# Optimization experiments

Measured on AMD Instinct MI355X. Metric: run time of the kernel, lower is better.

Reference implementation:

```python
import jax, jax.numpy as jnp
import numpy as np

B, T, N, C_IN = 8, 16, 2048, 2
H, C_OUT = 64, 64
KT, K = 3, 3
E = 32768


def setup_inputs() -> dict:
    key = jax.random.key(0)
    ks = jax.random.split(key, 8)
    X = jax.random.normal(ks[0], (B, T, N, C_IN), jnp.float32)
    edge_index = jax.random.randint(ks[1], (2, E), 0, N, dtype=jnp.int64)
    edge_weight = jax.random.uniform(ks[2], (E,), jnp.float32)
    conv1_w = jax.random.normal(ks[3], (2 * H, C_IN, KT, 1), jnp.float32) * 0.1
    conv1_b = jnp.zeros((2 * H,), jnp.float32)
    cheb_w = jax.random.normal(ks[4], (K, H, H), jnp.float32) * 0.05
    cheb_b = jnp.zeros((H,), jnp.float32)
    conv2_w = jax.random.normal(ks[5], (2 * C_OUT, H, KT, 1), jnp.float32) * 0.05
    conv2_b = jnp.zeros((2 * C_OUT,), jnp.float32)
    return dict(X=X, edge_index=edge_index, edge_weight=edge_weight,
                conv1_w=conv1_w, conv1_b=conv1_b, cheb_w=cheb_w, cheb_b=cheb_b,
                conv2_w=conv2_w, conv2_b=conv2_b)


def temporal_conv(x, w, b, c_out, kt):
    # x: [B, T, N, C_in] -> [B, T-kt+1, N, c_out]; causal conv (valid) + GLU with aligned residual
    xc = jnp.transpose(x, (0, 3, 1, 2))  # [B, C, T, N]
    bsz, c_in, t, n = xc.shape
    if c_in < c_out:
        x_in = jnp.concatenate([xc, jnp.zeros((bsz, c_out - c_in, t, n), xc.dtype)], axis=1)
    else:
        x_in = xc  # c_in == c_out case here (Align identity)
    x_in = x_in[:, :, kt - 1:, :]
    y = jax.lax.conv_general_dilated(xc, w, (1, 1), 'VALID',
                                     dimension_numbers=('NCHW', 'OIHW', 'NCHW'))
    y = y + b[None, :, None, None]  # [B, 2*c_out, T-kt+1, N]
    x_p, x_q = y[:, :c_out], y[:, c_out:]
    out = (x_p + x_in) * jax.nn.sigmoid(x_q)  # GLU
    return jnp.transpose(out, (0, 2, 3, 1))  # [B, T', N, c_out]


def cheb_conv(x, src, dst, ew, W, bias):
    # x: [G, N, H]. PyG ChebConv, sym normalization, lambda_max=2 =>
    # L_hat = -D^{-1/2} A D^{-1/2} with zero diagonal (self-loops removed/cancelled).
    n = x.shape[1]
    w = jnp.where(src == dst, jnp.zeros_like(ew), ew)  # remove self loops
    deg = jnp.zeros((n,), x.dtype).at[src].add(w)
    deg_safe = jnp.where(deg > 0, deg, jnp.ones_like(deg))
    dis = jnp.where(deg > 0, jax.lax.rsqrt(deg_safe), jnp.zeros_like(deg))
    wn = -dis[src] * w * dis[dst]  # scaled Laplacian edge weights

    def lhat(z):  # sparse L_hat @ z, batched over graph dim
        return jnp.zeros_like(z).at[:, dst].add(z[:, src] * wn[None, :, None])

    tx0 = x
    out = jnp.einsum('gnh,ho->gno', tx0, W[0])
    tx1 = lhat(x)
    out = out + jnp.einsum('gnh,ho->gno', tx1, W[1])
    for k in range(2, W.shape[0]):
        tx2 = 2.0 * lhat(tx1) - tx0
        out = out + jnp.einsum('gnh,ho->gno', tx2, W[k])
        tx0, tx1 = tx1, tx2
    return out + bias


def reference(X, edge_index, edge_weight, conv1_w, conv1_b, cheb_w, cheb_b, conv2_w, conv2_b):
    t0 = temporal_conv(X, conv1_w, conv1_b, H, KT)      # [B, T-2, N, H]
    bsz, tm, n, h = t0.shape
    g = t0.reshape(bsz * tm, n, h)
    src, dst = edge_index[0], edge_index[1]
    tg = cheb_conv(g, src, dst, edge_weight, cheb_w, cheb_b)
    tg = jax.nn.relu(tg).reshape(bsz, tm, n, h)
    out = temporal_conv(tg, conv2_w, conv2_b, C_OUT, KT)  # [B, T-4, N, C_OUT]
    # batch_norm=False, dropout=0 (eval): the permute pairs cancel -> identity
    return out
```

## Files before the change

kernel.cpp:

```cpp
#include <hip/hip_runtime.h>
#include <cstdint>

#define B_ 8
#define T_ 16
#define N_ 2048
#define CIN_ 2
#define H_ 64
#define COUT_ 64
#define KT_ 3
#define E_ 32768
#define T1_ 14
#define T2_ 12
#define G_ (B_*T1_)

typedef __attribute__((ext_vector_type(8))) short bf16x8;
typedef __attribute__((ext_vector_type(4))) float f32x4;
typedef unsigned short ushort_;
typedef __attribute__((ext_vector_type(8))) unsigned short u16x8;

__device__ __forceinline__ float sigmoidf_(float x){ return 1.f/(1.f+expf(-x)); }
__device__ __forceinline__ int rfl_(int x){ return __builtin_amdgcn_readfirstlane(x); }

__device__ __forceinline__ ushort_ f2b(float x){
  union {float f; uint32_t u;} v; v.f = x;
  uint32_t r = (v.u + 0x7FFFu + ((v.u>>16)&1u)) >> 16;
  return (ushort_)r;
}
__device__ __forceinline__ float b2f(ushort_ x){
  union {uint32_t u; float f;} v; v.u = ((uint32_t)x)<<16;
  return v.f;
}

__global__ void k_setup(const float* __restrict__ cw, const float* __restrict__ w2,
                        ushort_* __restrict__ Bp, ushort_* __restrict__ Bp2,
                        float* __restrict__ deg, int* __restrict__ cnt,
                        int* __restrict__ fillc){
  int bi = blockIdx.x; int tid = threadIdx.x;
  if(bi < 6){
    int i = bi*256 + tid;
    int lane = i & 63; int cn = i >> 6; int c = cn >> 2; int n = cn & 3;
    #pragma unroll
    for(int j=0;j<8;j++){
      int k = c*32 + (lane>>4)*8 + j;
      int h = k & 63; int m = k >> 6;
      int col = n*16 + (lane&15);
      float v;
      if(m == 0)      v = cw[(size_t)h*64 + col] - cw[(size_t)(128+h)*64 + col];
      else if(m == 1) v = cw[(size_t)(64+h)*64 + col];
      else            v = 2.f*cw[(size_t)(128+h)*64 + col];
      Bp[(size_t)i*8 + j] = f2b(v);
    }
  } else if(bi < 18){
    int i = (bi-6)*256 + tid;
    int lane = i & 63; int cn = i >> 6; int c = cn >> 3; int n = cn & 7;
    #pragma unroll
    for(int j=0;j<8;j++){
      int k = c*32 + (lane>>4)*8 + j;
      int co = n*16 + (lane&15);
      int kt = k >> 6, ci = k & 63;
      Bp2[(size_t)i*8 + j] = f2b(w2[(size_t)co*192 + ci*3 + kt]);
    }
  } else {
    int i = (bi-18)*256 + tid;
    if(i < N_){ deg[i] = 0.f; cnt[i] = 0; fillc[i] = 0; }
  }
}

__global__ void k_deg_cnt(const int* __restrict__ src, const int* __restrict__ dst,
                          const float* __restrict__ ew, float* deg, int* cnt){
  int e = blockIdx.x*blockDim.x + threadIdx.x;
  if(e >= E_) return;
  int s = src[e], d = dst[e];
  float w = (s==d) ? 0.f : ew[e];
  atomicAdd(&deg[s], w);
  atomicAdd(&cnt[d], 1);
}

__global__ void k_scan_dis(const int* __restrict__ cnt, int* __restrict__ offs,
                           float* __restrict__ deg){
  __shared__ int sums[256];
  int tid = threadIdx.x;
  int base = tid*8;
  int loc[8]; int s = 0;
  #pragma unroll
  for(int j=0;j<8;j++){ loc[j]=s; s += cnt[base+j]; }
  sums[tid] = s; __syncthreads();
  for(int ofs=1; ofs<256; ofs<<=1){
    int t = (tid>=ofs) ? sums[tid-ofs] : 0;
    __syncthreads();
    sums[tid] += t;
    __syncthreads();
  }
  int ebase = (tid==0) ? 0 : sums[tid-1];
  #pragma unroll
  for(int j=0;j<8;j++) offs[base+j] = ebase + loc[j];
  if(tid==255) offs[N_] = sums[255];
  #pragma unroll
  for(int j=0;j<8;j++){
    float dg = deg[base+j];
    deg[base+j] = dg > 0.f ? rsqrtf(dg) : 0.f;
  }
}

__global__ void k_fill_conv1(const int* __restrict__ src, const int* __restrict__ dst,
                             const float* __restrict__ ew, const float* __restrict__ dis,
                             const int* __restrict__ offs, int* fillc,
                             int2* __restrict__ epack,
                             const float* __restrict__ X, const float* __restrict__ w1,
                             const float* __restrict__ b1, ushort_* __restrict__ t0){
  int bi = blockIdx.x;
  if(bi < 128){
    int e = bi*256 + threadIdx.x;
    if(e >= E_) return;
    int s = src[e], d = dst[e];
    float w = (s==d) ? 0.f : ew[e];
    float wn = -dis[s]*w*dis[d];
    int pos = offs[d] + atomicAdd(&fillc[d], 1);
    epack[pos] = make_int2(s, __float_as_int(wn));
    return;
  }
  int wv = rfl_((bi-128)*4 + (threadIdx.x>>6));
  int lane = threadIdx.x & 63;
  int nb = wv % (N_/8); int bt = wv / (N_/8); int b = bt / T1_; int t = bt % T1_;
  int n0 = nb*8;
  const float* Xp = X + ((size_t)((b*T_ + t)*N_ + n0))*CIN_;
  float wp[6], wq[6];
  #pragma unroll
  for(int k=0;k<6;k++){
    wp[k] = w1[ lane      *6 + k];
    wq[k] = w1[(lane+H_)*6 + k];
  }
  float bp = b1[lane], bq = b1[lane+H_];
  ushort_* ob = t0 + ((size_t)bt*N_ + n0)*H_ + lane;
  #pragma unroll
  for(int j=0;j<8;j++){
    float yp = bp, yq = bq;
    #pragma unroll
    for(int kt=0;kt<KT_;kt++)
      #pragma unroll
      for(int ci=0;ci<CIN_;ci++){
        float x = Xp[kt*(N_*CIN_) + j*CIN_ + ci];
        yp += x * wp[ci*3+kt];
        yq += x * wq[ci*3+kt];
      }
    float xin = (lane < CIN_) ? Xp[2*(N_*CIN_) + j*CIN_ + lane] : 0.f;
    ob[j*H_] = f2b((yp + xin) * sigmoidf_(yq));
  }
}

__global__ void k_spmm3(const ushort_* __restrict__ zin, ushort_* __restrict__ out,
                        const int* __restrict__ offs, const int2* __restrict__ epack){
  int lane = threadIdx.x & 63;
  int wv = threadIdx.x >> 6;
  int bid = blockIdx.x;
  int work = (bid & 7)*896 + (bid >> 3);
  int gg = work >> 9;
  int dblk = work & 511;
  int d = dblk*4 + wv;
  int e0 = offs[d], e1 = offs[d+1];
  size_t lbase = (size_t)(gg*8 + (lane>>3))*N_*H_ + (lane&7)*8;
  const ushort_* zb = zin + lbase;
  float ac[8] = {};
  int i = e0;
  for(; i+7 < e1; i += 8){
    int2 ee[8]; u16x8 zz[8];
    #pragma unroll
    for(int u=0;u<8;u++) ee[u] = epack[i+u];
    #pragma unroll
    for(int u=0;u<8;u++) zz[u] = *(const u16x8*)(zb + (size_t)ee[u].x*H_);
    #pragma unroll
    for(int u=0;u<8;u++){
      float w = __int_as_float(ee[u].y);
      #pragma unroll
      for(int j=0;j<8;j++) ac[j] += w*b2f(zz[u][j]);
    }
  }
  for(; i+3 < e1; i += 4){
    int2 ee[4]; u16x8 zz[4];
    #pragma unroll
    for(int u=0;u<4;u++) ee[u] = epack[i+u];
    #pragma unroll
    for(int u=0;u<4;u++) zz[u] = *(const u16x8*)(zb + (size_t)ee[u].x*H_);
    #pragma unroll
    for(int u=0;u<4;u++){
      float w = __int_as_float(ee[u].y);
      #pragma unroll
      for(int j=0;j<8;j++) ac[j] += w*b2f(zz[u][j]);
    }
  }
  for(; i < e1; i++){
    int2 e = epack[i];
    float w = __int_as_float(e.y);
    u16x8 zv = *(const u16x8*)(zb + (size_t)e.x*H_);
    #pragma unroll
    for(int j=0;j<8;j++) ac[j] += w*b2f(zv[j]);
  }
  u16x8 ov;
  #pragma unroll
  for(int j=0;j<8;j++) ov[j] = f2b(ac[j]);
  *(u16x8*)(out + lbase + (size_t)d*H_) = ov;
}

__global__ __launch_bounds__(256) void k_cheb_mfma(
    const ushort_* __restrict__ t0, const ushort_* __restrict__ tx1,
    const ushort_* __restrict__ y2, const ushort_* __restrict__ Bp,
    const float* __restrict__ bias, ushort_* __restrict__ tg){
  __shared__ ushort_ lb[6*4*64*8];
  int tid = threadIdx.x;
  #pragma unroll
  for(int i=0;i<6;i++)
    *(u16x8*)(lb + i*2048 + tid*8) = *(const u16x8*)(Bp + i*2048 + tid*8);
  __syncthreads();
  int lane = tid & 63;
  int wv = tid >> 6;
  int bid = blockIdx.x;
  int xcd = bid & 7;
  int local = bid >> 3;
  int g = xcd*14 + (local >> 4);
  int row0 = (local & 15)*128 + wv*32;
  int ra = row0 + (lane&15);
  bf16x8 a[2][6];
  #pragma unroll
  for(int c=0;c<6;c++){
    const ushort_* s = (c>>1)==0 ? t0 : ((c>>1)==1 ? tx1 : y2);
    int eoff = (c&1)*32 + (lane>>4)*8;
    const ushort_* sb = s + (size_t)g*N_*H_ + eoff;
    a[0][c] = *(const bf16x8*)(sb + (size_t)ra*H_);
    a[1][c] = *(const bf16x8*)(sb + (size_t)(ra+16)*H_);
  }
  f32x4 acc[2][4] = {};
  #pragma unroll
  for(int c=0;c<6;c++){
    #pragma unroll
    for(int n=0;n<4;n++){
      bf16x8 bfr = *(const bf16x8*)(lb + ((c*4+n)*64 + lane)*8);
      acc[0][n] = __builtin_amdgcn_mfma_f32_16x16x32_bf16(a[0][c], bfr, acc[0][n], 0,0,0);
      acc[1][n] = __builtin_amdgcn_mfma_f32_16x16x32_bf16(a[1][c], bfr, acc[1][n], 0,0,0);
    }
  }
  #pragma unroll
  for(int rg=0; rg<2; rg++)
    #pragma unroll
    for(int n=0;n<4;n++){
      int col = n*16 + (lane&15);
      float bv = bias[col];
      #pragma unroll
      for(int r=0;r<4;r++){
        int row = row0 + rg*16 + (lane>>4)*4 + r;
        float v = fmaxf(acc[rg][n][r] + bv, 0.f);
        tg[(size_t)(g*N_+row)*H_ + col] = f2b(v);
      }
    }
}

__global__ __launch_bounds__(256) void k_conv2_mfma(
    const ushort_* __restrict__ tg, const ushort_* __restrict__ Bp2,
    const float* __restrict__ b2, float* __restrict__ out){
  __shared__ ushort_ lb[6*8*64*8];
  int tid = threadIdx.x;
  #pragma unroll
  for(int i=0;i<12;i++)
    *(u16x8*)(lb + i*2048 + tid*8) = *(const u16x8*)(Bp2 + i*2048 + tid*8);
  __syncthreads();
  int lane = tid & 63;
  int wv = tid >> 6;
  int bid = blockIdx.x;
  int b = bid & 7;
  int local = bid >> 3;
  int t = local >> 4; int nblk = local & 15;
  int n0 = nblk*128 + wv*32;
  const ushort_* base = tg + (size_t)(b*T1_ + t)*N_*H_;
  int ra = n0 + (lane&15);
  f32x4 acc[2][8] = {};
  #pragma unroll
  for(int c=0;c<6;c++){
    const ushort_* s = base + (size_t)(c>>1)*N_*H_;
    int eoff = (c&1)*32 + (lane>>4)*8;
    bf16x8 a0 = *(const bf16x8*)(s + (size_t)ra*H_ + eoff);
    bf16x8 a1 = *(const bf16x8*)(s + (size_t)(ra+16)*H_ + eoff);
    #pragma unroll
    for(int n=0;n<8;n++){
      bf16x8 bfr = *(const bf16x8*)(lb + ((c*8+n)*64 + lane)*8);
      acc[0][n] = __builtin_amdgcn_mfma_f32_16x16x32_bf16(a0, bfr, acc[0][n], 0,0,0);
      acc[1][n] = __builtin_amdgcn_mfma_f32_16x16x32_bf16(a1, bfr, acc[1][n], 0,0,0);
    }
  }
  const ushort_* xslab = base + (size_t)2*N_*H_;
  float* ob = out + (size_t)(b*T2_ + t)*N_*H_;
  #pragma unroll
  for(int rg=0;rg<2;rg++)
    #pragma unroll
    for(int n=0;n<4;n++){
      int col = n*16 + (lane&15);
      float bp = b2[col], bq = b2[col+COUT_];
      #pragma unroll
      for(int r=0;r<4;r++){
        int row = n0 + rg*16 + (lane>>4)*4 + r;
        float xin = b2f(xslab[(size_t)row*H_ + col]);
        float p = acc[rg][n][r] + bp + xin;
        float q = acc[rg][n+4][r] + bq;
        ob[(size_t)row*H_ + col] = p * sigmoidf_(q);
      }
    }
}

extern "C" void kernel_launch(void* const* d_in, const int* in_sizes, int n_in,
                              void* d_out, int out_size, void* d_ws, size_t ws_size,
                              hipStream_t stream){
  (void)in_sizes; (void)n_in; (void)out_size; (void)ws_size;
  const float* X  = (const float*)d_in[0];
  const int*   ei = (const int*)d_in[1];
  const float* ew = (const float*)d_in[2];
  const float* w1 = (const float*)d_in[3];
  const float* b1 = (const float*)d_in[4];
  const float* cw = (const float*)d_in[5];
  const float* cb = (const float*)d_in[6];
  const float* w2 = (const float*)d_in[7];
  const float* b2 = (const float*)d_in[8];
  float* out = (float*)d_out;

  char* ws = (char*)d_ws;
  const size_t BUF = (size_t)G_*N_*H_*sizeof(ushort_);
  ushort_* t0  = (ushort_*)(ws);
  ushort_* tx1 = (ushort_*)(ws + BUF);
  ushort_* y2  = (ushort_*)(ws + 2*BUF);
  ushort_* tg  = (ushort_*)(ws + 3*BUF);
  char* sm = ws + 4*BUF;
  float* deg   = (float*)(sm);
  int*   cnt   = (int*)  (sm + 8192);
  int*   fillc = (int*)  (sm + 16384);
  int*   offs  = (int*)  (sm + 24576);
  int2*  epack = (int2*) (sm + 33024);
  ushort_* Bp  = (ushort_*)(sm + 33024 + 262144);
  ushort_* Bp2 = (ushort_*)(sm + 33024 + 262144 + 24576);

  const int* src = ei;
  const int* dst = ei + E_;

  k_setup   <<<26,     256, 0, stream>>>(cw, w2, Bp, Bp2, deg, cnt, fillc);
  k_deg_cnt <<<E_/256, 256, 0, stream>>>(src, dst, ew, deg, cnt);
  k_scan_dis<<<1,      256, 0, stream>>>(cnt, offs, deg);

  k_fill_conv1<<<128 + (G_*N_/8)/4, 256, 0, stream>>>(
      src, dst, ew, deg, offs, fillc, epack, X, w1, b1, t0);

  k_spmm3<<<14*512, 256, 0, stream>>>(t0,  tx1, offs, epack);
  k_spmm3<<<14*512, 256, 0, stream>>>(tx1, y2,  offs, epack);

  k_cheb_mfma<<<G_*16, 256, 0, stream>>>(t0, tx1, y2, Bp, cb, tg);

  k_conv2_mfma<<<(B_*T2_)*16, 256, 0, stream>>>(tg, Bp2, b2, out);
}
```

Measured before the change: 148.5 us.

## Fuse setup, degree, scan and fill/conv1 into one cooperative kernel

```diff
diff --git a/kernel.cpp b/kernel.cpp
--- a/kernel.cpp
+++ b/kernel.cpp
@@ -1,5 +1,8 @@
 #include <hip/hip_runtime.h>
+#include <hip/hip_cooperative_groups.h>
 #include <cstdint>
+
+namespace cg = cooperative_groups;
 
 #define B_ 8
 #define T_ 16
@@ -31,120 +34,122 @@
   return v.f;
 }
 
-__global__ void k_setup(const float* __restrict__ cw, const float* __restrict__ w2,
-                        ushort_* __restrict__ Bp, ushort_* __restrict__ Bp2,
+#define CONV1_BLKS 448
+__global__ void k_front(const int* __restrict__ src, const int* __restrict__ dst,
+                        const float* __restrict__ ew, const float* __restrict__ X,
+                        const float* __restrict__ w1, const float* __restrict__ b1,
+                        const float* __restrict__ cw, const float* __restrict__ w2,
                         float* __restrict__ deg, int* __restrict__ cnt,
-                        int* __restrict__ fillc){
+                        int* __restrict__ fillc, int* __restrict__ offs,
+                        int2* __restrict__ epack, ushort_* __restrict__ Bp,
+                        ushort_* __restrict__ Bp2, ushort_* __restrict__ t0){
+  cg::grid_group grid = cg::this_grid();
+  __shared__ int sums[256];
   int bi = blockIdx.x; int tid = threadIdx.x;
-  if(bi < 6){
-    int i = bi*256 + tid;
-    int lane = i & 63; int cn = i >> 6; int c = cn >> 2; int n = cn & 3;
-    #pragma unroll
-    for(int j=0;j<8;j++){
-      int k = c*32 + (lane>>4)*8 + j;
-      int h = k & 63; int m = k >> 6;
-      int col = n*16 + (lane&15);
-      float v;
-      if(m == 0)      v = cw[(size_t)h*64 + col] - cw[(size_t)(128+h)*64 + col];
-      else if(m == 1) v = cw[(size_t)(64+h)*64 + col];
-      else            v = 2.f*cw[(size_t)(128+h)*64 + col];
-      Bp[(size_t)i*8 + j] = f2b(v);
-    }
-  } else if(bi < 18){
-    int i = (bi-6)*256 + tid;
-    int lane = i & 63; int cn = i >> 6; int c = cn >> 3; int n = cn & 7;
-    #pragma unroll
-    for(int j=0;j<8;j++){
-      int k = c*32 + (lane>>4)*8 + j;
-      int co = n*16 + (lane&15);
-      int kt = k >> 6, ci = k & 63;
-      Bp2[(size_t)i*8 + j] = f2b(w2[(size_t)co*192 + ci*3 + kt]);
-    }
-  } else {
-    int i = (bi-18)*256 + tid;
-    if(i < N_){ deg[i] = 0.f; cnt[i] = 0; fillc[i] = 0; }
-  }
-}
-
-__global__ void k_deg_cnt(const int* __restrict__ src, const int* __restrict__ dst,
-                          const float* __restrict__ ew, float* deg, int* cnt){
-  int e = blockIdx.x*blockDim.x + threadIdx.x;
-  if(e >= E_) return;
-  int s = src[e], d = dst[e];
-  float w = (s==d) ? 0.f : ew[e];
-  atomicAdd(&deg[s], w);
-  atomicAdd(&cnt[d], 1);
-}
-
-__global__ void k_scan_dis(const int* __restrict__ cnt, int* __restrict__ offs,
-                           float* __restrict__ deg){
-  __shared__ int sums[256];
-  int tid = threadIdx.x;
-  int base = tid*8;
-  int loc[8]; int s = 0;
-  #pragma unroll
-  for(int j=0;j<8;j++){ loc[j]=s; s += cnt[base+j]; }
-  sums[tid] = s; __syncthreads();
-  for(int ofs=1; ofs<256; ofs<<=1){
-    int t = (tid>=ofs) ? sums[tid-ofs] : 0;
-    __syncthreads();
-    sums[tid] += t;
-    __syncthreads();
-  }
-  int ebase = (tid==0) ? 0 : sums[tid-1];
-  #pragma unroll
-  for(int j=0;j<8;j++) offs[base+j] = ebase + loc[j];
-  if(tid==255) offs[N_] = sums[255];
-  #pragma unroll
-  for(int j=0;j<8;j++){
-    float dg = deg[base+j];
-    deg[base+j] = dg > 0.f ? rsqrtf(dg) : 0.f;
-  }
-}
-
-__global__ void k_fill_conv1(const int* __restrict__ src, const int* __restrict__ dst,
-                             const float* __restrict__ ew, const float* __restrict__ dis,
-                             const int* __restrict__ offs, int* fillc,
-                             int2* __restrict__ epack,
-                             const float* __restrict__ X, const float* __restrict__ w1,
-                             const float* __restrict__ b1, ushort_* __restrict__ t0){
-  int bi = blockIdx.x;
+
+  if(bi >= 128 && bi < 154){
+    int sb = bi - 128;
+    if(sb < 6){
+      int i = sb*256 + tid;
+      int lane = i & 63; int cn = i >> 6; int c = cn >> 2; int n = cn & 3;
+      #pragma unroll
+      for(int j=0;j<8;j++){
+        int k = c*32 + (lane>>4)*8 + j;
+        int h = k & 63; int m = k >> 6;
+        int col = n*16 + (lane&15);
+        float v;
+        if(m == 0)      v = cw[(size_t)h*64 + col] - cw[(size_t)(128+h)*64 + col];
+        else if(m == 1) v = cw[(size_t)(64+h)*64 + col];
+        else            v = 2.f*cw[(size_t)(128+h)*64 + col];
+        Bp[(size_t)i*8 + j] = f2b(v);
+      }
+    } else if(sb < 18){
+      int i = (sb-6)*256 + tid;
+      int lane = i & 63; int cn = i >> 6; int c = cn >> 3; int n = cn & 7;
+      #pragma unroll
+      for(int j=0;j<8;j++){
+        int k = c*32 + (lane>>4)*8 + j;
+        int co = n*16 + (lane&15);
+        int kt = k >> 6, ci = k & 63;
+        Bp2[(size_t)i*8 + j] = f2b(w2[(size_t)co*192 + ci*3 + kt]);
+      }
+    } else {
+      int i = (sb-18)*256 + tid;
+      if(i < N_){ deg[i] = 0.f; cnt[i] = 0; fillc[i] = 0; }
+    }
+  } else if(bi >= 154){
+    int lane = tid & 63;
+    float wp[6], wq[6];
+    #pragma unroll
+    for(int k=0;k<6;k++){
+      wp[k] = w1[ lane      *6 + k];
+      wq[k] = w1[(lane+H_)*6 + k];
+    }
+    float bp = b1[lane], bq = b1[lane+H_];
+    for(int wv = (bi-154)*4 + (tid>>6); wv < G_*N_/8; wv += CONV1_BLKS*4){
+      int wvu = rfl_(wv);
+      int nb = wvu % (N_/8); int bt = wvu / (N_/8); int b = bt / T1_; int t = bt % T1_;
+      int n0 = nb*8;
+      const float* Xp = X + ((size_t)((b*T_ + t)*N_ + n0))*CIN_;
+      ushort_* ob = t0 + ((size_t)bt*N_ + n0)*H_ + lane;
+      #pragma unroll
+      for(int j=0;j<8;j++){
+        float yp = bp, yq = bq;
+        #pragma unroll
+        for(int kt=0;kt<KT_;kt++)
+          #pragma unroll
+          for(int ci=0;ci<CIN_;ci++){
+            float x = Xp[kt*(N_*CIN_) + j*CIN_ + ci];
+            yp += x * wp[ci*3+kt];
+            yq += x * wq[ci*3+kt];
+          }
+        float xin = (lane < CIN_) ? Xp[2*(N_*CIN_) + j*CIN_ + lane] : 0.f;
+        ob[j*H_] = f2b((yp + xin) * sigmoidf_(yq));
+      }
+    }
+  }
+  grid.sync();
+
   if(bi < 128){
-    int e = bi*256 + threadIdx.x;
-    if(e >= E_) return;
+    int e = bi*256 + tid;
     int s = src[e], d = dst[e];
     float w = (s==d) ? 0.f : ew[e];
-    float wn = -dis[s]*w*dis[d];
+    atomicAdd(&deg[s], w);
+    atomicAdd(&cnt[d], 1);
+  }
+  grid.sync();
+
+  if(bi == 0){
+    int base = tid*8;
+    int loc[8]; int s = 0;
+    #pragma unroll
+    for(int j=0;j<8;j++){ loc[j]=s; s += cnt[base+j]; }
+    sums[tid] = s; __syncthreads();
+    for(int ofs=1; ofs<256; ofs<<=1){
+      int t = (tid>=ofs) ? sums[tid-ofs] : 0;
+      __syncthreads();
+      sums[tid] += t;
+      __syncthreads();
+    }
+    int ebase = (tid==0) ? 0 : sums[tid-1];
+    #pragma unroll
+    for(int j=0;j<8;j++) offs[base+j] = ebase + loc[j];
+    if(tid==255) offs[N_] = sums[255];
+    #pragma unroll
+    for(int j=0;j<8;j++){
+      float dg = deg[base+j];
+      deg[base+j] = dg > 0.f ? rsqrtf(dg) : 0.f;
+    }
+  }
+  grid.sync();
+
+  if(bi < 128){
+    int e = bi*256 + tid;
+    int s = src[e], d = dst[e];
+    float w = (s==d) ? 0.f : ew[e];
+    float wn = -deg[s]*w*deg[d];
     int pos = offs[d] + atomicAdd(&fillc[d], 1);
     epack[pos] = make_int2(s, __float_as_int(wn));
-    return;
-  }
-  int wv = rfl_((bi-128)*4 + (threadIdx.x>>6));
-  int lane = threadIdx.x & 63;
-  int nb = wv % (N_/8); int bt = wv / (N_/8); int b = bt / T1_; int t = bt % T1_;
-  int n0 = nb*8;
-  const float* Xp = X + ((size_t)((b*T_ + t)*N_ + n0))*CIN_;
-  float wp[6], wq[6];
-  #pragma unroll
-  for(int k=0;k<6;k++){
-    wp[k] = w1[ lane      *6 + k];
-    wq[k] = w1[(lane+H_)*6 + k];
-  }
-  float bp = b1[lane], bq = b1[lane+H_];
-  ushort_* ob = t0 + ((size_t)bt*N_ + n0)*H_ + lane;
-  #pragma unroll
-  for(int j=0;j<8;j++){
-    float yp = bp, yq = bq;
-    #pragma unroll
-    for(int kt=0;kt<KT_;kt++)
-      #pragma unroll
-      for(int ci=0;ci<CIN_;ci++){
-        float x = Xp[kt*(N_*CIN_) + j*CIN_ + ci];
-        yp += x * wp[ci*3+kt];
-        yq += x * wq[ci*3+kt];
-      }
-    float xin = (lane < CIN_) ? Xp[2*(N_*CIN_) + j*CIN_ + lane] : 0.f;
-    ob[j*H_] = f2b((yp + xin) * sigmoidf_(yq));
   }
 }
 
@@ -337,12 +342,12 @@
   const int* src = ei;
   const int* dst = ei + E_;
 
-  k_setup   <<<26,     256, 0, stream>>>(cw, w2, Bp, Bp2, deg, cnt, fillc);
-  k_deg_cnt <<<E_/256, 256, 0, stream>>>(src, dst, ew, deg, cnt);
-  k_scan_dis<<<1,      256, 0, stream>>>(cnt, offs, deg);
-
-  k_fill_conv1<<<128 + (G_*N_/8)/4, 256, 0, stream>>>(
-      src, dst, ew, deg, offs, fillc, epack, X, w1, b1, t0);
+  void* args[] = {(void*)&src, (void*)&dst, (void*)&ew, (void*)&X,
+                  (void*)&w1, (void*)&b1, (void*)&cw, (void*)&w2,
+                  (void*)&deg, (void*)&cnt, (void*)&fillc, (void*)&offs,
+                  (void*)&epack, (void*)&Bp, (void*)&Bp2, (void*)&t0};
+  hipLaunchCooperativeKernel((void*)k_front, dim3(128 + 26 + CONV1_BLKS),
+                             dim3(256), args, 0, stream);
 
   k_spmm3<<<14*512, 256, 0, stream>>>(t0,  tx1, offs, epack);
   k_spmm3<<<14*512, 256, 0, stream>>>(tx1, y2,  offs, epack);
```

Result: slower. 368.8 us (+148.4%).
